# Performance work log

Measured on AMD Instinct MI355X. Metric: run time of the kernel, lower is better.

Reference implementation:

```python
import jax, jax.numpy as jnp
import numpy as np
from jax import lax

B, D, L = 32, 768, 512          # batch, embedding_dim, max_sent_len
H, R, W = 1024, 20, 3            # hidden_dim, rel_size, window_size
P, S = 4096, 16                  # total entity pairs, max span length


def setup_inputs():
    key = jax.random.key(0)
    ks = jax.random.split(key, 16)
    sc = 0.02
    inp = {
        'rel_word_x': jax.random.normal(ks[0], (B, D, L), jnp.float32),
        'pair_batch': jax.random.randint(ks[1], (P,), 0, B),
        'head_index': jax.random.randint(ks[2], (P,), 0, L - S),
        'head_span':  jax.random.randint(ks[3], (P,), 1, S + 1),
        'tail_index': jax.random.randint(ks[4], (P,), 0, L - S),
        'tail_span':  jax.random.randint(ks[5], (P,), 1, S + 1),
        'rel_labels': jax.random.randint(ks[6], (P,), 0, R),
        # learned params (PyTorch layouts: Conv1d [O,I,K], Linear [out,in])
        'conv1_w': jax.random.normal(ks[7], (D, D, W), jnp.float32) * sc,
        'conv1_b': jnp.zeros((D,), jnp.float32),
        'conv2_w': jax.random.normal(ks[8], (D, D, W), jnp.float32) * sc,
        'conv2_b': jnp.zeros((D,), jnp.float32),
        'lin1_w': jax.random.normal(ks[9], (H, D), jnp.float32) * sc,
        'lin1_b': jnp.zeros((H,), jnp.float32),
        'lin2_w': jax.random.normal(ks[10], (H, H), jnp.float32) * sc,
        'lin2_b': jnp.zeros((H,), jnp.float32),
        'rel_w': jax.random.normal(ks[11], (R, H), jnp.float32) * sc,
        'rel_b': jnp.zeros((R,), jnp.float32),
    }
    return inp


def _conv1d(x, w, b):
    # x: [B, D, L], w: [O, I, K] -> [B, O, L] (same padding)
    y = lax.conv_general_dilated(x, w, (1,), [(W // 2, W // 2)],
                                 dimension_numbers=('NCH', 'OIH', 'NCH'))
    return y + b[None, :, None]


def _span_max(x_t, batch, idx, span):
    # x_t: [B, L, D]; returns [P, D] max-pool over each variable-length span
    pos = jnp.minimum(idx[:, None] + jnp.arange(S), L - 1)        # [P, S]
    feats = x_t[batch[:, None], pos]                               # [P, S, D]
    mask = (jnp.arange(S)[None, :] < span[:, None])[:, :, None]    # [P, S, 1]
    return jnp.max(jnp.where(mask, feats, -jnp.inf), axis=1)


def reference(rel_word_x, pair_batch, head_index, head_span, tail_index,
              tail_span, rel_labels, conv1_w, conv1_b, conv2_w, conv2_b,
              lin1_w, lin1_b, lin2_w, lin2_b, rel_w, rel_b):
    # dropout layers are identity (eval mode) for a deterministic reference
    x = rel_word_x
    x = jax.nn.relu(_conv1d(x, conv1_w, conv1_b)) + x
    x = jax.nn.relu(_conv1d(x, conv2_w, conv2_b)) + x
    x_t = jnp.transpose(x, (0, 2, 1))                              # [B, L, D]

    headrep = _span_max(x_t, pair_batch, head_index, head_span)    # [P, D]
    tailrep = _span_max(x_t, pair_batch, tail_index, tail_span)    # [P, D]
    maxed = headrep + tailrep
    maxed = jax.nn.relu(maxed @ lin1_w.T + lin1_b)                 # [P, H]
    maxed = jax.nn.relu(maxed @ lin2_w.T + lin2_b)                 # [P, H]
    rel_logits = maxed @ rel_w.T + rel_b                           # [P, R]
    return rel_logits, rel_labels
```

## Files before the change

### kernel.cpp

```cpp
#include <hip/hip_runtime.h>


#define B_  32
#define D_  768
#define L_  512
#define LP_ 514
#define H_  1024
#define R_  20
#define P_  4096
#define K1_ 2304

typedef __attribute__((ext_vector_type(8))) short sh8;
typedef __attribute__((ext_vector_type(4))) short sh4;
typedef __attribute__((ext_vector_type(4))) float f32x4;

__device__ __forceinline__ float bf2f(unsigned short u) {
  union { unsigned u; float f; } c; c.u = ((unsigned)u) << 16; return c.f;
}
__device__ __forceinline__ unsigned short f2bf(float f) {
  union { float f; unsigned u; } c; c.f = f;
  unsigned u = c.u + 0x7fffu + ((c.u >> 16) & 1u);
  return (unsigned short)(u >> 16);
}
__device__ __forceinline__ void gld16(const void* g, void* l) {
  __builtin_amdgcn_global_load_lds((const __attribute__((address_space(1))) void*)g,
                                   (__attribute__((address_space(3))) void*)l,
                                   16, 0, 0);
}

__global__ void transpose_pad_kernel(const float* __restrict__ x,
                                     unsigned short* __restrict__ xpad) {
  __shared__ float tile[32][33];
  const int b = blockIdx.z;
  const int l0 = blockIdx.x * 32, d0 = blockIdx.y * 32;
  const int tx = threadIdx.x, ty = threadIdx.y;
#pragma unroll
  for (int r = 0; r < 4; ++r)
    tile[ty + r * 8][tx] = x[((size_t)b * D_ + d0 + ty + r * 8) * L_ + l0 + tx];
  __syncthreads();
#pragma unroll
  for (int r = 0; r < 4; ++r) {
    int l = l0 + ty + r * 8, d = d0 + tx;
    xpad[((size_t)b * LP_ + 1 + l) * D_ + d] = f2bf(tile[tx][ty + r * 8]);
  }
}

__global__ void zero_pad_kernel(unsigned short* __restrict__ xp0,
                                unsigned short* __restrict__ xp1) {
  int i = blockIdx.x * 256 + threadIdx.x;
  int b = i / D_, d = i % D_;
  size_t r0 = (size_t)b * LP_ * D_ + d;
  size_t r1 = ((size_t)b * LP_ + (LP_ - 1)) * D_ + d;
  xp0[r0] = 0; xp0[r1] = 0; xp1[r0] = 0; xp1[r1] = 0;
}

__global__ void prep_w_kernel(const float* __restrict__ w1, const float* __restrict__ w2,
                              const float* __restrict__ l1, const float* __restrict__ l2,
                              unsigned short* __restrict__ wt1, unsigned short* __restrict__ wt2,
                              unsigned short* __restrict__ l1b, unsigned short* __restrict__ l2b) {
  int i = blockIdx.x * 256 + threadIdx.x;
  const int CW = D_ * D_ * 3;
  if (i < CW) {
    int o = i / (3 * D_), rem = i % (3 * D_);
    int k = rem / D_, c = rem % D_;
    int src = (o * D_ + c) * 3 + k;
    wt1[i] = f2bf(w1[src]);
    wt2[i] = f2bf(w2[src]);
  }
  if (i < H_ * D_) l1b[i] = f2bf(l1[i]);
  if (i < H_ * H_) l2b[i] = f2bf(l2[i]);
}

template<bool APAD, bool RESIDUAL, bool OUTPAD>
__global__ __launch_bounds__(256)
void gemm_kernel(const unsigned short* __restrict__ A, int lda,
                 const unsigned short* __restrict__ Bw, int K,
                 const float* __restrict__ bias,
                 const unsigned short* __restrict__ res,
                 unsigned short* __restrict__ outb, int ldo) {
  __shared__ unsigned short Atile[3][128 * 32];
  __shared__ unsigned short Btile[3][128 * 32];

  const int tid  = threadIdx.x;
  const int wave = tid >> 6;
  const int lane = tid & 63;
  const int wr = wave >> 1, wc = wave & 1;

  const int nwg  = gridDim.x * gridDim.y;
  const int orig = blockIdx.y * gridDim.x + blockIdx.x;
  int bswz = orig;
  if ((nwg & 7) == 0) bswz = (orig & 7) * (nwg >> 3) + (orig >> 3);
  const int m0 = (bswz / gridDim.x) * 128;
  const int n0 = (bswz % gridDim.x) * 128;

  int arow0;
  if (APAD) arow0 = (m0 >> 9) * LP_ + (m0 & 511);
  else      arow0 = m0;

  f32x4 acc[4][4];
#pragma unroll
  for (int i = 0; i < 4; ++i)
#pragma unroll
    for (int j = 0; j < 4; ++j) acc[i][j] = (f32x4)(0.0f);

  const int srow = lane >> 2;
  const int scol = (lane & 3) * 8;
  const int l16 = lane & 15, lq = lane >> 4;

  const unsigned short* Ab = A + (size_t)arow0 * lda + scol;
  const unsigned short* Bb = Bw + (size_t)n0 * K + scol;
  const int c0 = wave * 2, c1 = wave * 2 + 1;
  const int rowA0 = c0 * 16 + srow, rowA1 = c1 * 16 + srow;

#define STAGE(buf, kk) do {                                          \
    gld16(Ab + (size_t)rowA0 * lda + (kk), &Atile[buf][c0 * 512]);   \
    gld16(Bb + (size_t)rowA0 * K   + (kk), &Btile[buf][c0 * 512]);   \
    gld16(Ab + (size_t)rowA1 * lda + (kk), &Atile[buf][c1 * 512]);   \
    gld16(Bb + (size_t)rowA1 * K   + (kk), &Btile[buf][c1 * 512]);   \
  } while (0)

  const int nIter = K >> 5;
  STAGE(0, 0);
  STAGE(1, 32);

  int cur = 0;
  for (int t = 0; t < nIter; ++t) {
    if (t + 1 < nIter) asm volatile("s_waitcnt vmcnt(4)" ::: "memory");
    else               asm volatile("s_waitcnt vmcnt(0)" ::: "memory");
    __builtin_amdgcn_s_barrier();

    sh8 af[4], bfr[4];
#pragma unroll
    for (int i = 0; i < 4; ++i)
      af[i] = *(const sh8*)&Atile[cur][(wr * 64 + i * 16 + l16) * 32 + lq * 8];
#pragma unroll
    for (int j = 0; j < 4; ++j)
      bfr[j] = *(const sh8*)&Btile[cur][(wc * 64 + j * 16 + l16) * 32 + lq * 8];

    if (t + 2 < nIter) {
      int sb = cur + 2; if (sb >= 3) sb -= 3;
      STAGE(sb, (t + 2) * 32);
    }

#pragma unroll
    for (int i = 0; i < 4; ++i)
#pragma unroll
      for (int j = 0; j < 4; ++j)
        acc[i][j] = __builtin_amdgcn_mfma_f32_16x16x32_bf16(af[i], bfr[j], acc[i][j], 0, 0, 0);

    cur = (cur == 2) ? 0 : cur + 1;
  }
#undef STAGE

#pragma unroll
  for (int i = 0; i < 4; ++i) {
#pragma unroll
    for (int j = 0; j < 4; ++j) {
      int col = n0 + wc * 64 + j * 16 + l16;
      float bn = bias[col];
#pragma unroll
      for (int r = 0; r < 4; ++r) {
        int m = m0 + wr * 64 + i * 16 + lq * 4 + r;
        float v = acc[i][j][r] + bn;
        v = fmaxf(v, 0.0f);
        size_t orow = (size_t)m;
        if (OUTPAD || RESIDUAL) {
          int bb = m >> 9, ll = m & 511;
          size_t prow = (size_t)bb * LP_ + ll + 1;
          if (RESIDUAL) v += bf2f(res[prow * D_ + col]);
          if (OUTPAD) orow = prow;
        }
        outb[orow * (size_t)ldo + col] = f2bf(v);
      }
    }
  }
}

__global__ void span_kernel(const unsigned short* __restrict__ x2,
                            const int* __restrict__ pb, const int* __restrict__ hi,
                            const int* __restrict__ hs, const int* __restrict__ ti,
                            const int* __restrict__ ts,
                            unsigned short* __restrict__ maxed) {
  const int p = blockIdx.x, t = threadIdx.x;
  const int b = pb[p];
  const unsigned short* xb = x2 + (size_t)b * L_ * D_ + t * 4;

  float mh[4], mt[4];
#pragma unroll
  for (int j = 0; j < 4; ++j) { mh[j] = -1e30f; mt[j] = -1e30f; }
  {
    int idx = hi[p], sp = hs[p];
    for (int s = 0; s < sp; ++s) {
      int pos = idx + s; if (pos > L_ - 1) pos = L_ - 1;
      sh4 v = *(const sh4*)(xb + (size_t)pos * D_);
#pragma unroll
      for (int j = 0; j < 4; ++j) mh[j] = fmaxf(mh[j], bf2f((unsigned short)v[j]));
    }
  }
  {
    int idx = ti[p], sp = ts[p];
    for (int s = 0; s < sp; ++s) {
      int pos = idx + s; if (pos > L_ - 1) pos = L_ - 1;
      sh4 v = *(const sh4*)(xb + (size_t)pos * D_);
#pragma unroll
      for (int j = 0; j < 4; ++j) mt[j] = fmaxf(mt[j], bf2f((unsigned short)v[j]));
    }
  }
  sh4 o;
#pragma unroll
  for (int j = 0; j < 4; ++j) o[j] = (short)f2bf(mh[j] + mt[j]);
  *(sh4*)(maxed + (size_t)p * D_ + t * 4) = o;
}

__global__ void rel_kernel(const unsigned short* __restrict__ h2,
                           const float* __restrict__ rw, const float* __restrict__ rb,
                           const int* __restrict__ labels, float* __restrict__ out) {
  const int wave = threadIdx.x >> 6, lane = threadIdx.x & 63;
  const int p = blockIdx.x * 4 + wave;
  float a[16];
#pragma unroll
  for (int j = 0; j < 16; ++j) a[j] = bf2f(h2[(size_t)p * H_ + lane + j * 64]);
  for (int r = 0; r < R_; ++r) {
    float s = 0.f;
    const float* wrow = rw + (size_t)r * H_;
#pragma unroll
    for (int j = 0; j < 16; ++j) s += a[j] * wrow[lane + j * 64];
#pragma unroll
    for (int m = 32; m >= 1; m >>= 1) s += __shfl_xor(s, m);
    if (lane == 0) out[(size_t)p * R_ + r] = s + rb[r];
  }
  if (threadIdx.x < 4) {
    int pp = blockIdx.x * 4 + threadIdx.x;
    out[(size_t)P_ * R_ + pp] = (float)labels[pp];
  }
}

extern "C" void kernel_launch(void* const* d_in, const int* in_sizes, int n_in,
                              void* d_out, int out_size, void* d_ws, size_t ws_size,
                              hipStream_t stream) {
  const float* x      = (const float*)d_in[0];
  const int*   pb     = (const int*)d_in[1];
  const int*   hi     = (const int*)d_in[2];
  const int*   hs     = (const int*)d_in[3];
  const int*   ti     = (const int*)d_in[4];
  const int*   ts     = (const int*)d_in[5];
  const int*   labels = (const int*)d_in[6];
  const float* w1     = (const float*)d_in[7];
  const float* b1     = (const float*)d_in[8];
  const float* w2     = (const float*)d_in[9];
  const float* b2     = (const float*)d_in[10];
  const float* l1w    = (const float*)d_in[11];
  const float* l1bias = (const float*)d_in[12];
  const float* l2w    = (const float*)d_in[13];
  const float* l2bias = (const float*)d_in[14];
  const float* rw     = (const float*)d_in[15];
  const float* rbias  = (const float*)d_in[16];
  float* out = (float*)d_out;

  unsigned short* ws    = (unsigned short*)d_ws;
  unsigned short* xpad0 = ws;
  unsigned short* xpad1 = xpad0 + (size_t)B_ * LP_ * D_;
  unsigned short* x2    = xpad1 + (size_t)B_ * LP_ * D_;
  unsigned short* wt1   = x2    + (size_t)B_ * L_ * D_;
  unsigned short* wt2   = wt1   + (size_t)D_ * 3 * D_;
  unsigned short* l1b   = wt2   + (size_t)D_ * 3 * D_;
  unsigned short* l2b   = l1b   + (size_t)H_ * D_;
  unsigned short* maxed = xpad0;
  unsigned short* h1    = xpad0 + (size_t)P_ * D_;
  unsigned short* h2    = h1    + (size_t)P_ * H_;

  transpose_pad_kernel<<<dim3(L_ / 32, D_ / 32, B_), dim3(32, 8, 1), 0, stream>>>(x, xpad0);
  zero_pad_kernel<<<(B_ * D_) / 256, 256, 0, stream>>>(xpad0, xpad1);
  prep_w_kernel<<<(D_ * D_ * 3) / 256, 256, 0, stream>>>(w1, w2, l1w, l2w, wt1, wt2, l1b, l2b);

  gemm_kernel<true, true, true><<<dim3(D_ / 128, (B_ * L_) / 128), 256, 0, stream>>>(
      xpad0, D_, wt1, K1_, b1, xpad0, xpad1, D_);
  gemm_kernel<true, true, false><<<dim3(D_ / 128, (B_ * L_) / 128), 256, 0, stream>>>(
      xpad1, D_, wt2, K1_, b2, xpad1, x2, D_);

  span_kernel<<<P_, 192, 0, stream>>>(x2, pb, hi, hs, ti, ts, maxed);

  gemm_kernel<false, false, false><<<dim3(H_ / 128, P_ / 128), 256, 0, stream>>>(
      maxed, D_, l1b, D_, l1bias, nullptr, h1, H_);
  gemm_kernel<false, false, false><<<dim3(H_ / 128, P_ / 128), 256, 0, stream>>>(
      h1, H_, l2b, H_, l2bias, nullptr, h2, H_);

  rel_kernel<<<P_ / 4, 256, 0, stream>>>(h2, rw, rbias, labels, out);
}
```

Before: 366.0 us.

## Swizzle GEMM LDS tiles, fuse pad zeroing, sort spans by batch, restructure weight prep

Applies an XOR swizzle to the 16-byte column chunks in the GEMM LDS tiles, on both the global-to-LDS store side and the fragment reads, to reduce LDS bank conflicts. Folds the zero-padding kernel into the transpose kernel. Reworks weight preparation so each thread handles one (o,c) pair across the three taps. Adds a counting sort of pairs by batch index and spreads sorted blocks across XCD-style slots so span gathers hit the same batch in cache. This saves launches and conflicts but adds a single-block sort kernel launch, and perm reuses the wt1 buffer after the conv GEMMs.

```diff
diff --git a/kernel.cpp b/kernel.cpp
--- a/kernel.cpp
+++ b/kernel.cpp
@@ -29,7 +29,8 @@
 }
 
 __global__ void transpose_pad_kernel(const float* __restrict__ x,
-                                     unsigned short* __restrict__ xpad) {
+                                     unsigned short* __restrict__ xpad,
+                                     unsigned short* __restrict__ xpad1) {
   __shared__ float tile[32][33];
   const int b = blockIdx.z;
   const int l0 = blockIdx.x * 32, d0 = blockIdx.y * 32;
@@ -37,21 +38,17 @@
 #pragma unroll
   for (int r = 0; r < 4; ++r)
     tile[ty + r * 8][tx] = x[((size_t)b * D_ + d0 + ty + r * 8) * L_ + l0 + tx];
+  if (l0 == 0 && ty < 4) {
+    size_t row = (ty & 1) ? ((size_t)b * LP_ + LP_ - 1) * D_ : (size_t)b * LP_ * D_;
+    unsigned short* dst = (ty < 2) ? xpad : xpad1;
+    dst[row + d0 + tx] = 0;
+  }
   __syncthreads();
 #pragma unroll
   for (int r = 0; r < 4; ++r) {
     int l = l0 + ty + r * 8, d = d0 + tx;
     xpad[((size_t)b * LP_ + 1 + l) * D_ + d] = f2bf(tile[tx][ty + r * 8]);
   }
-}
-
-__global__ void zero_pad_kernel(unsigned short* __restrict__ xp0,
-                                unsigned short* __restrict__ xp1) {
-  int i = blockIdx.x * 256 + threadIdx.x;
-  int b = i / D_, d = i % D_;
-  size_t r0 = (size_t)b * LP_ * D_ + d;
-  size_t r1 = ((size_t)b * LP_ + (LP_ - 1)) * D_ + d;
-  xp0[r0] = 0; xp0[r1] = 0; xp1[r0] = 0; xp1[r1] = 0;
 }
 
 __global__ void prep_w_kernel(const float* __restrict__ w1, const float* __restrict__ w2,
@@ -59,13 +56,16 @@
                               unsigned short* __restrict__ wt1, unsigned short* __restrict__ wt2,
                               unsigned short* __restrict__ l1b, unsigned short* __restrict__ l2b) {
   int i = blockIdx.x * 256 + threadIdx.x;
-  const int CW = D_ * D_ * 3;
-  if (i < CW) {
-    int o = i / (3 * D_), rem = i % (3 * D_);
-    int k = rem / D_, c = rem % D_;
-    int src = (o * D_ + c) * 3 + k;
-    wt1[i] = f2bf(w1[src]);
-    wt2[i] = f2bf(w2[src]);
+  if (i < D_ * D_) {
+    int o = i / D_, c = i % D_;
+    const float* s1 = w1 + (size_t)i * 3;
+    const float* s2 = w2 + (size_t)i * 3;
+    size_t dbase = (size_t)o * 3 * D_ + c;
+#pragma unroll
+    for (int k = 0; k < 3; ++k) {
+      wt1[dbase + (size_t)k * D_] = f2bf(s1[k]);
+      wt2[dbase + (size_t)k * D_] = f2bf(s2[k]);
+    }
   }
   if (i < H_ * D_) l1b[i] = f2bf(l1[i]);
   if (i < H_ * H_) l2b[i] = f2bf(l2[i]);
@@ -104,8 +104,9 @@
     for (int j = 0; j < 4; ++j) acc[i][j] = (f32x4)(0.0f);
 
   const int srow = lane >> 2;
-  const int scol = (lane & 3) * 8;
+  const int scol = (((lane & 3) ^ ((lane >> 2) & 3)) * 8);
   const int l16 = lane & 15, lq = lane >> 4;
+  const int lsw = (lq ^ (l16 & 3)) * 8;
 
   const unsigned short* Ab = A + (size_t)arow0 * lda + scol;
   const unsigned short* Bb = Bw + (size_t)n0 * K + scol;
@@ -132,10 +133,10 @@
     sh8 af[4], bfr[4];
 #pragma unroll
     for (int i = 0; i < 4; ++i)
-      af[i] = *(const sh8*)&Atile[cur][(wr * 64 + i * 16 + l16) * 32 + lq * 8];
+      af[i] = *(const sh8*)&Atile[cur][(wr * 64 + i * 16 + l16) * 32 + lsw];
 #pragma unroll
     for (int j = 0; j < 4; ++j)
-      bfr[j] = *(const sh8*)&Btile[cur][(wc * 64 + j * 16 + l16) * 32 + lq * 8];
+      bfr[j] = *(const sh8*)&Btile[cur][(wc * 64 + j * 16 + l16) * 32 + lsw];
 
     if (t + 2 < nIter) {
       int sb = cur + 2; if (sb >= 3) sb -= 3;
@@ -176,12 +177,33 @@
   }
 }
 
+__global__ void span_sort_kernel(const int* __restrict__ pb, int* __restrict__ perm) {
+  __shared__ int cnt[B_], off[B_];
+  const int t = threadIdx.x;
+  if (t < B_) cnt[t] = 0;
+  __syncthreads();
+  int bv[4];
+#pragma unroll
+  for (int r = 0; r < 4; ++r) { bv[r] = pb[t * 4 + r]; atomicAdd(&cnt[bv[r]], 1); }
+  __syncthreads();
+  if (t == 0) { int s = 0; for (int i = 0; i < B_; ++i) { off[i] = s; s += cnt[i]; } }
+  __syncthreads();
+#pragma unroll
+  for (int r = 0; r < 4; ++r) {
+    int pos = atomicAdd(&off[bv[r]], 1);
+    perm[pos] = t * 4 + r;
+  }
+}
+
 __global__ void span_kernel(const unsigned short* __restrict__ x2,
+                            const int* __restrict__ perm,
                             const int* __restrict__ pb, const int* __restrict__ hi,
                             const int* __restrict__ hs, const int* __restrict__ ti,
                             const int* __restrict__ ts,
                             unsigned short* __restrict__ maxed) {
-  const int p = blockIdx.x, t = threadIdx.x;
+  const int sidx = (blockIdx.x & 7) * (P_ / 8) + (blockIdx.x >> 3);
+  const int p = perm[sidx];
+  const int t = threadIdx.x;
   const int b = pb[p];
   const unsigned short* xb = x2 + (size_t)b * L_ * D_ + t * 4;
 
@@ -268,17 +290,18 @@
   unsigned short* maxed = xpad0;
   unsigned short* h1    = xpad0 + (size_t)P_ * D_;
   unsigned short* h2    = h1    + (size_t)P_ * H_;
-
-  transpose_pad_kernel<<<dim3(L_ / 32, D_ / 32, B_), dim3(32, 8, 1), 0, stream>>>(x, xpad0);
-  zero_pad_kernel<<<(B_ * D_) / 256, 256, 0, stream>>>(xpad0, xpad1);
-  prep_w_kernel<<<(D_ * D_ * 3) / 256, 256, 0, stream>>>(w1, w2, l1w, l2w, wt1, wt2, l1b, l2b);
+  int* perm = (int*)wt1;
+
+  transpose_pad_kernel<<<dim3(L_ / 32, D_ / 32, B_), dim3(32, 8, 1), 0, stream>>>(x, xpad0, xpad1);
+  prep_w_kernel<<<(H_ * H_) / 256, 256, 0, stream>>>(w1, w2, l1w, l2w, wt1, wt2, l1b, l2b);
 
   gemm_kernel<true, true, true><<<dim3(D_ / 128, (B_ * L_) / 128), 256, 0, stream>>>(
       xpad0, D_, wt1, K1_, b1, xpad0, xpad1, D_);
   gemm_kernel<true, true, false><<<dim3(D_ / 128, (B_ * L_) / 128), 256, 0, stream>>>(
       xpad1, D_, wt2, K1_, b2, xpad1, x2, D_);
 
-  span_kernel<<<P_, 192, 0, stream>>>(x2, pb, hi, hs, ti, ts, maxed);
+  span_sort_kernel<<<1, 1024, 0, stream>>>(pb, perm);
+  span_kernel<<<P_, 192, 0, stream>>>(x2, perm, pb, hi, hs, ti, ts, maxed);
 
   gemm_kernel<false, false, false><<<dim3(H_ / 128, P_ / 128), 256, 0, stream>>>(
       maxed, D_, l1b, D_, l1bias, nullptr, h1, H_);
```

Result: no change. 361.2 us (-1.3%).
